# Kernel tuning notes

Measured on AMD Instinct MI355X. Metric: run time of the kernel, lower is better.

Reference implementation:

```python
import jax, jax.numpy as jnp
import numpy as np

N_NODES = 50000
N_EDGES = 800000
D_IN = 128
D_OUT = 128


def setup_inputs() -> dict:
    key = jax.random.key(0)
    k1, k2, k3, k4, k5 = jax.random.split(key, 5)
    x = jax.random.normal(k1, (N_NODES, D_IN), dtype=jnp.float32)
    w = jax.random.normal(k2, (D_IN, D_OUT), dtype=jnp.float32) * (1.0 / np.sqrt(D_IN))
    adj_rows = jnp.sort(jax.random.randint(k3, (N_EDGES,), 0, N_NODES, dtype=jnp.int32))
    adj_cols = jax.random.randint(k4, (N_EDGES,), 0, N_NODES, dtype=jnp.int32)
    adj_vals = jax.random.uniform(k5, (N_EDGES,), dtype=jnp.float32)
    return {"x": x, "w": w, "adj_rows": adj_rows, "adj_cols": adj_cols, "adj_vals": adj_vals}


def reference(x, w, adj_rows, adj_cols, adj_vals):
    # dense feature transform: [N, D_in] @ [D_in, D_out] -> [N, D_out]
    h = jnp.matmul(x, w)
    # sparse adjacency propagation (SpMM in COO form):
    # out[r] = sum over edges (r, c, v) of v * h[c]
    msg = adj_vals[:, None] * h[adj_cols]          # [E, D_out] gather
    out = jax.ops.segment_sum(msg, adj_rows, num_segments=x.shape[0])
    # activation (relu), fused into output pass
    return jax.nn.relu(out)
```

## Files before the change

### kernel.cpp

```cpp
#include <hip/hip_runtime.h>
#include <hip/hip_bf16.h>

#define D 128
#define GEMM_ROWS 32

typedef __bf16 bf16x8 __attribute__((ext_vector_type(8)));
typedef float  f32x4  __attribute__((ext_vector_type(4)));
typedef float  f32x2  __attribute__((ext_vector_type(2)));
typedef unsigned int u32x4 __attribute__((ext_vector_type(4)));

__device__ inline bf16x8 cvt_a8(const float* __restrict__ p) {
    float4 v0 = ((const float4*)p)[0], v1 = ((const float4*)p)[1];
    bf16x8 a;
    a[0] = (__bf16)v0.x; a[1] = (__bf16)v0.y; a[2] = (__bf16)v0.z; a[3] = (__bf16)v0.w;
    a[4] = (__bf16)v1.x; a[5] = (__bf16)v1.y; a[6] = (__bf16)v1.z; a[7] = (__bf16)v1.w;
    return a;
}

__global__ __launch_bounds__(256) void fused_gemm_rp(
        const float* __restrict__ x, const float* __restrict__ w,
        const int* __restrict__ rows,
        unsigned short* __restrict__ h, int* __restrict__ rp,
        int n_nodes, int n_edges, int gemm_blocks) {
    const int b = blockIdx.x;

    if (b >= gemm_blocks) {
        int e = (b - gemm_blocks) * 256 + threadIdx.x;
        if (e >= n_edges) return;
        int r    = rows[e];
        int prev = (e == 0) ? -1 : rows[e - 1];
        for (int rr = prev + 1; rr <= r; ++rr) rp[rr] = e;
        if (e == n_edges - 1)
            for (int rr = r + 1; rr <= n_nodes; ++rr) rp[rr] = n_edges;
        return;
    }

    const int wave = threadIdx.x >> 6;
    const int lane = threadIdx.x & 63;
    const int m16  = lane & 15;
    const int q    = lane >> 4;

    const int row0 = b * 64;
    const int col0 = wave * 32;

    bf16x8 bfr[2][4];
#pragma unroll
    for (int t = 0; t < 2; ++t)
#pragma unroll
        for (int s = 0; s < 4; ++s) {
            const float* wp = w + (size_t)(32 * s + q * 8) * D + col0 + 16 * t + m16;
#pragma unroll
            for (int j = 0; j < 8; ++j)
                bfr[t][s][j] = (__bf16)wp[(size_t)j * D];
        }

#pragma unroll 1
    for (int sl = 0; sl < 4; ++sl) {
        const int r = row0 + sl * 16 + m16;
        const float* xp = x + (size_t)r * D + q * 8;

        bf16x8 a[4];
        if (r < n_nodes) {
#pragma unroll
            for (int s = 0; s < 4; ++s) a[s] = cvt_a8(xp + 32 * s);
        } else {
#pragma unroll
            for (int s = 0; s < 4; ++s)
#pragma unroll
                for (int j = 0; j < 8; ++j) a[s][j] = (__bf16)0.f;
        }

        f32x4 acc0 = (f32x4)0.f, acc1 = (f32x4)0.f;
#pragma unroll
        for (int s = 0; s < 4; ++s) {
            acc0 = __builtin_amdgcn_mfma_f32_16x16x32_bf16(a[s], bfr[0][s], acc0, 0, 0, 0);
            acc1 = __builtin_amdgcn_mfma_f32_16x16x32_bf16(a[s], bfr[1][s], acc1, 0, 0, 0);
        }

#pragma unroll
        for (int i = 0; i < 4; ++i) {
            int row = row0 + sl * 16 + q * 4 + i;
            h[(size_t)row * D + col0 + m16]      = __builtin_bit_cast(unsigned short, (__bf16)acc0[i]);
            h[(size_t)row * D + col0 + 16 + m16] = __builtin_bit_cast(unsigned short, (__bf16)acc1[i]);
        }
    }
}

#define PKFMA(hv, vv)                                                          \
    _Pragma("unroll")                                                          \
    for (int j = 0; j < 4; ++j) {                                              \
        unsigned int u = (hv)[j];                                              \
        f32x2 f;                                                               \
        f[0] = __builtin_bit_cast(float, u << 16);                             \
        f[1] = __builtin_bit_cast(float, u & 0xFFFF0000u);                     \
        acc2[j] = __builtin_elementwise_fma((f32x2)(vv), f, acc2[j]);          \
    }

__global__ __launch_bounds__(256) void spmm_bf16_pk(
        const unsigned short* __restrict__ h,
        const int* __restrict__ row_ptr,
        const int* __restrict__ cols,
        const float* __restrict__ vals,
        float* __restrict__ out, int n) {
    const int wave = threadIdx.x >> 6;
    const int lane = threadIdx.x & 63;
    const int r = blockIdx.x * 4 + wave;
    if (r >= n) return;

    const int start = row_ptr[r];
    const int end   = row_ptr[r + 1];
    const int chain = lane >> 4;
    const int l4    = lane & 15;

    const u32x4* h4 = (const u32x4*)h;
    f32x2 acc2[4];
#pragma unroll
    for (int j = 0; j < 4; ++j) acc2[j] = (f32x2)0.f;

    const int last = end - 1;
    int e = start + chain;
    while (e < end) {
        int i1 = (e + 4  <= last) ? e + 4  : last;
        int i2 = (e + 8  <= last) ? e + 8  : last;
        int i3 = (e + 12 <= last) ? e + 12 : last;
        int   c0 = cols[e],  c1 = cols[i1], c2 = cols[i2], c3 = cols[i3];
        float v0 = vals[e];
        float v1 = (e + 4  < end) ? vals[i1] : 0.f;
        float v2 = (e + 8  < end) ? vals[i2] : 0.f;
        float v3 = (e + 12 < end) ? vals[i3] : 0.f;

        u32x4 hv0 = h4[(size_t)c0 * (D / 8) + l4];
        u32x4 hv1 = h4[(size_t)c1 * (D / 8) + l4];
        u32x4 hv2 = h4[(size_t)c2 * (D / 8) + l4];
        u32x4 hv3 = h4[(size_t)c3 * (D / 8) + l4];

        PKFMA(hv0, v0)
        PKFMA(hv1, v1)
        PKFMA(hv2, v2)
        PKFMA(hv3, v3)

        e += 16;
    }

#pragma unroll
    for (int j = 0; j < 4; ++j) {
#pragma unroll
        for (int k = 0; k < 2; ++k) {
            float a = acc2[j][k];
            a += __shfl_xor(a, 16);
            a += __shfl_xor(a, 32);
            acc2[j][k] = a;
        }
    }

    if (chain == 0) {
        float4 o0, o1;
        o0.x = fmaxf(acc2[0][0], 0.f); o0.y = fmaxf(acc2[0][1], 0.f);
        o0.z = fmaxf(acc2[1][0], 0.f); o0.w = fmaxf(acc2[1][1], 0.f);
        o1.x = fmaxf(acc2[2][0], 0.f); o1.y = fmaxf(acc2[2][1], 0.f);
        o1.z = fmaxf(acc2[3][0], 0.f); o1.w = fmaxf(acc2[3][1], 0.f);
        float4* op = (float4*)(out + (size_t)r * D + l4 * 8);
        op[0] = o0; op[1] = o1;
    }
}

__global__ __launch_bounds__(256) void gemm128(const float* __restrict__ x,
                                               const float* __restrict__ w,
                                               float* __restrict__ h, int n) {
    __shared__ float4 ws4[D * D / 4];
    __shared__ float  xs[GEMM_ROWS][D];
    const int tid  = threadIdx.x;
    const int row0 = blockIdx.x * GEMM_ROWS;
    const float4* w4 = (const float4*)w;
    for (int i = tid; i < D * D / 4; i += 256) ws4[i] = w4[i];
    float4* xs4 = (float4*)&xs[0][0];
    const float4* x4 = (const float4*)x;
    for (int i = tid; i < GEMM_ROWS * D / 4; i += 256) {
        int row = row0 + (i >> 5);
        float4 v = make_float4(0.f, 0.f, 0.f, 0.f);
        if (row < n) v = x4[(size_t)row0 * (D / 4) + i];
        xs4[i] = v;
    }
    __syncthreads();
    const int tx = tid & 31, ty = tid >> 5;
    float4 acc[4];
#pragma unroll
    for (int i = 0; i < 4; ++i) acc[i] = make_float4(0.f, 0.f, 0.f, 0.f);
#pragma unroll 8
    for (int k = 0; k < D; ++k) {
        float4 wv = ws4[k * (D / 4) + tx];
#pragma unroll
        for (int i = 0; i < 4; ++i) {
            float xv = xs[ty * 4 + i][k];
            acc[i].x = fmaf(xv, wv.x, acc[i].x);
            acc[i].y = fmaf(xv, wv.y, acc[i].y);
            acc[i].z = fmaf(xv, wv.z, acc[i].z);
            acc[i].w = fmaf(xv, wv.w, acc[i].w);
        }
    }
#pragma unroll
    for (int i = 0; i < 4; ++i) {
        int row = row0 + ty * 4 + i;
        if (row < n) ((float4*)(h + (size_t)row * D))[tx] = acc[i];
    }
}

__global__ __launch_bounds__(128) void spmm_row(const float* __restrict__ h,
                                                const int* __restrict__ rows,
                                                const int* __restrict__ cols,
                                                const float* __restrict__ vals,
                                                float* __restrict__ out, int n_edges) {
    const int r = blockIdx.x, d = threadIdx.x;
    int lo = 0, hi = n_edges;
    while (lo < hi) { int m = (lo + hi) >> 1; if (rows[m] < r) lo = m + 1; else hi = m; }
    const int start = lo;
    hi = n_edges;
    while (lo < hi) { int m = (lo + hi) >> 1; if (rows[m] <= r) lo = m + 1; else hi = m; }
    const int end = lo;
    float acc = 0.f;
    for (int e = start; e < end; ++e)
        acc = fmaf(vals[e], h[(size_t)cols[e] * D + d], acc);
    out[(size_t)r * D + d] = fmaxf(acc, 0.f);
}

__global__ __launch_bounds__(128) void fused_fallback(
        const float* __restrict__ x, const float* __restrict__ w,
        const int* __restrict__ rows, const int* __restrict__ cols,
        const float* __restrict__ vals, float* __restrict__ out, int n_edges) {
    const int r = blockIdx.x, d = threadIdx.x;
    int lo = 0, hi = n_edges;
    while (lo < hi) { int m = (lo + hi) >> 1; if (rows[m] < r) lo = m + 1; else hi = m; }
    const int start = lo;
    hi = n_edges;
    while (lo < hi) { int m = (lo + hi) >> 1; if (rows[m] <= r) lo = m + 1; else hi = m; }
    const int end = lo;
    float acc = 0.f;
    for (int e = start; e < end; ++e) {
        int c = cols[e]; float v = vals[e];
        float hcd = 0.f;
        for (int k = 0; k < D; ++k)
            hcd = fmaf(x[(size_t)c * D + k], w[(size_t)k * D + d], hcd);
        acc = fmaf(v, hcd, acc);
    }
    out[(size_t)r * D + d] = fmaxf(acc, 0.f);
}

extern "C" void kernel_launch(void* const* d_in, const int* in_sizes, int n_in,
                              void* d_out, int out_size, void* d_ws, size_t ws_size,
                              hipStream_t stream) {
    const float* x    = (const float*)d_in[0];
    const float* w    = (const float*)d_in[1];
    const int*   rows = (const int*)d_in[2];
    const int*   cols = (const int*)d_in[3];
    const float* vals = (const float*)d_in[4];
    float* out = (float*)d_out;

    const int n_nodes = in_sizes[0] / D;
    const int n_edges = in_sizes[2];
    const int n_pad   = (n_nodes + 63) & ~63;

    const size_t h_bytes  = (size_t)n_pad * D * sizeof(unsigned short);
    const size_t rp_off   = h_bytes;
    const size_t need     = rp_off + (size_t)(n_nodes + 1) * sizeof(int);
    const size_t hf_bytes = (size_t)n_nodes * D * sizeof(float);

    if (ws_size >= need) {
        unsigned short* h  = (unsigned short*)d_ws;
        int*            rp = (int*)((char*)d_ws + rp_off);

        const int gemm_blocks = n_pad / 64;
        const int rp_blocks   = (n_edges + 255) / 256;
        fused_gemm_rp<<<gemm_blocks + rp_blocks, 256, 0, stream>>>(
            x, w, rows, h, rp, n_nodes, n_edges, gemm_blocks);

        spmm_bf16_pk<<<(n_nodes + 3) / 4, 256, 0, stream>>>(h, rp, cols, vals, out, n_nodes);
    } else if (ws_size >= hf_bytes) {
        float* hf = (float*)d_ws;
        gemm128<<<(n_nodes + GEMM_ROWS - 1) / GEMM_ROWS, 256, 0, stream>>>(x, w, hf, n_nodes);
        spmm_row<<<n_nodes, 128, 0, stream>>>(hf, rows, cols, vals, out, n_edges);
    } else {
        fused_fallback<<<n_nodes, 128, 0, stream>>>(x, w, rows, cols, vals, out, n_edges);
    }
}
```

Baseline: 127.0 us.

## Split h into column slabs mapped to XCDs for L2-local SpMM gathers

The GEMM now writes h as four 32-column slabs (one per wave), each [n_pad,32] bf16. The SpMM kernel maps block indices so each column slab is handled by a fixed pair of XCDs, and each wave processes 4 rows with 16 edge chains of 4 lanes each. The aim is to shrink the gathered working set per XCD (a 3.2 MB slab instead of 12.8 MB) so random h gathers hit in the per-XCD L2. In exchange, each row's cols/vals are read four times and each gather is only 64 bytes, with extra shuffle reductions.

Result: slower. 168.8 us (+32.9%).

```diff
diff --git a/kernel.cpp b/kernel.cpp
--- a/kernel.cpp
+++ b/kernel.cpp
@@ -21,7 +21,7 @@
         const float* __restrict__ x, const float* __restrict__ w,
         const int* __restrict__ rows,
         unsigned short* __restrict__ h, int* __restrict__ rp,
-        int n_nodes, int n_edges, int gemm_blocks) {
+        int n_nodes, int n_pad, int n_edges, int gemm_blocks) {
     const int b = blockIdx.x;
 
     if (b >= gemm_blocks) {
@@ -80,8 +80,9 @@
 #pragma unroll
         for (int i = 0; i < 4; ++i) {
             int row = row0 + sl * 16 + q * 4 + i;
-            h[(size_t)row * D + col0 + m16]      = __builtin_bit_cast(unsigned short, (__bf16)acc0[i]);
-            h[(size_t)row * D + col0 + 16 + m16] = __builtin_bit_cast(unsigned short, (__bf16)acc1[i]);
+            unsigned short* hw = h + ((size_t)wave * n_pad + row) * 32;
+            hw[m16]      = __builtin_bit_cast(unsigned short, (__bf16)acc0[i]);
+            hw[16 + m16] = __builtin_bit_cast(unsigned short, (__bf16)acc1[i]);
         }
     }
 }
@@ -96,71 +97,75 @@
         acc2[j] = __builtin_elementwise_fma((f32x2)(vv), f, acc2[j]);          \
     }
 
-__global__ __launch_bounds__(256) void spmm_bf16_pk(
+__global__ __launch_bounds__(256) void spmm_bf16_xcd(
         const unsigned short* __restrict__ h,
         const int* __restrict__ row_ptr,
         const int* __restrict__ cols,
         const float* __restrict__ vals,
-        float* __restrict__ out, int n) {
+        float* __restrict__ out, int n, int n_pad) {
     const int wave = threadIdx.x >> 6;
     const int lane = threadIdx.x & 63;
-    const int r = blockIdx.x * 4 + wave;
-    if (r >= n) return;
-
-    const int start = row_ptr[r];
-    const int end   = row_ptr[r + 1];
-    const int chain = lane >> 4;
-    const int l4    = lane & 15;
-
-    const u32x4* h4 = (const u32x4*)h;
-    f32x2 acc2[4];
-#pragma unroll
-    for (int j = 0; j < 4; ++j) acc2[j] = (f32x2)0.f;
-
-    const int last = end - 1;
-    int e = start + chain;
-    while (e < end) {
-        int i1 = (e + 4  <= last) ? e + 4  : last;
-        int i2 = (e + 8  <= last) ? e + 8  : last;
-        int i3 = (e + 12 <= last) ? e + 12 : last;
-        int   c0 = cols[e],  c1 = cols[i1], c2 = cols[i2], c3 = cols[i3];
-        float v0 = vals[e];
-        float v1 = (e + 4  < end) ? vals[i1] : 0.f;
-        float v2 = (e + 8  < end) ? vals[i2] : 0.f;
-        float v3 = (e + 12 < end) ? vals[i3] : 0.f;
-
-        u32x4 hv0 = h4[(size_t)c0 * (D / 8) + l4];
-        u32x4 hv1 = h4[(size_t)c1 * (D / 8) + l4];
-        u32x4 hv2 = h4[(size_t)c2 * (D / 8) + l4];
-        u32x4 hv3 = h4[(size_t)c3 * (D / 8) + l4];
-
-        PKFMA(hv0, v0)
-        PKFMA(hv1, v1)
-        PKFMA(hv2, v2)
-        PKFMA(hv3, v3)
-
-        e += 16;
-    }
-
-#pragma unroll
-    for (int j = 0; j < 4; ++j) {
-#pragma unroll
-        for (int k = 0; k < 2; ++k) {
-            float a = acc2[j][k];
-            a += __shfl_xor(a, 16);
-            a += __shfl_xor(a, 32);
-            acc2[j][k] = a;
-        }
-    }
-
-    if (chain == 0) {
-        float4 o0, o1;
-        o0.x = fmaxf(acc2[0][0], 0.f); o0.y = fmaxf(acc2[0][1], 0.f);
-        o0.z = fmaxf(acc2[1][0], 0.f); o0.w = fmaxf(acc2[1][1], 0.f);
-        o1.x = fmaxf(acc2[2][0], 0.f); o1.y = fmaxf(acc2[2][1], 0.f);
-        o1.z = fmaxf(acc2[3][0], 0.f); o1.w = fmaxf(acc2[3][1], 0.f);
-        float4* op = (float4*)(out + (size_t)r * D + l4 * 8);
-        op[0] = o0; op[1] = o1;
+    const int b    = blockIdx.x;
+    const int s    = (b & 7) >> 1;
+    const int g    = (b >> 3) * 2 + (b & 1);
+    const int rbeg = (g * 4 + wave) * 4;
+    if (rbeg >= n) return;
+
+    const int echain = lane >> 2;
+    const int sub    = lane & 3;
+    const unsigned short* hs = h + (size_t)s * n_pad * 32;
+
+    const int rend = (rbeg + 4 < n) ? rbeg + 4 : n;
+#pragma unroll 1
+    for (int r = rbeg; r < rend; ++r) {
+        const int start = row_ptr[r];
+        const int end   = row_ptr[r + 1];
+
+        f32x2 acc2[4];
+#pragma unroll
+        for (int j = 0; j < 4; ++j) acc2[j] = (f32x2)0.f;
+
+        const int last = end - 1;
+#pragma unroll 1
+        for (int e = start; e < end; e += 32) {
+            int e0 = e + echain, e1 = e + 16 + echain;
+            int i0 = (e0 <= last) ? e0 : last;
+            int i1 = (e1 <= last) ? e1 : last;
+            int   c0 = cols[i0];
+            int   c1 = cols[i1];
+            float v0 = (e0 < end) ? vals[i0] : 0.f;
+            float v1 = (e1 < end) ? vals[i1] : 0.f;
+
+            u32x4 hv0 = *(const u32x4*)(hs + (size_t)c0 * 32 + sub * 8);
+            u32x4 hv1 = *(const u32x4*)(hs + (size_t)c1 * 32 + sub * 8);
+
+            PKFMA(hv0, v0)
+            PKFMA(hv1, v1)
+        }
+
+#pragma unroll
+        for (int j = 0; j < 4; ++j) {
+#pragma unroll
+            for (int k = 0; k < 2; ++k) {
+                float a = acc2[j][k];
+                a += __shfl_xor(a, 4);
+                a += __shfl_xor(a, 8);
+                a += __shfl_xor(a, 16);
+                a += __shfl_xor(a, 32);
+                acc2[j][k] = a;
+            }
+        }
+
+        if (echain == 0) {
+            float4 o0, o1;
+            o0.x = fmaxf(acc2[0][0], 0.f); o0.y = fmaxf(acc2[0][1], 0.f);
+            o0.z = fmaxf(acc2[1][0], 0.f); o0.w = fmaxf(acc2[1][1], 0.f);
+            o1.x = fmaxf(acc2[2][0], 0.f); o1.y = fmaxf(acc2[2][1], 0.f);
+            o1.z = fmaxf(acc2[3][0], 0.f); o1.w = fmaxf(acc2[3][1], 0.f);
+            float* op = out + (size_t)r * D + s * 32 + sub * 8;
+            ((float4*)op)[0] = o0;
+            ((float4*)op)[1] = o1;
+        }
     }
 }
 
@@ -271,9 +276,13 @@
         const int gemm_blocks = n_pad / 64;
         const int rp_blocks   = (n_edges + 255) / 256;
         fused_gemm_rp<<<gemm_blocks + rp_blocks, 256, 0, stream>>>(
-            x, w, rows, h, rp, n_nodes, n_edges, gemm_blocks);
-
-        spmm_bf16_pk<<<(n_nodes + 3) / 4, 256, 0, stream>>>(h, rp, cols, vals, out, n_nodes);
+            x, w, rows, h, rp, n_nodes, n_pad, n_edges, gemm_blocks);
+
+        const int waves_per_slab  = (n_nodes + 3) / 4;
+        int blocks_per_slab = (waves_per_slab + 3) / 4;
+        blocks_per_slab = (blocks_per_slab + 1) & ~1;
+        const int nb = blocks_per_slab * 4;
+        spmm_bf16_xcd<<<nb, 256, 0, stream>>>(h, rp, cols, vals, out, n_nodes, n_pad);
     } else if (ws_size >= hf_bytes) {
         float* hf = (float*)d_ws;
         gemm128<<<(n_nodes + GEMM_ROWS - 1) / GEMM_ROWS, 256, 0, stream>>>(x, w, hf, n_nodes);
```
